# Optimization experiments

Hardware: AMD Instinct MI355X
Metric: run time of the kernel (lower is better)

## Reference

```python
import jax, jax.numpy as jnp
import numpy as np

THETA = 10000.0
D_K = 128
MAX_SEQ_LEN = 4096
BATCH, HEADS, SEQ = 4, 16, 4096


def _create_rotation_matrix(theta, d_k, max_seq_len):
    # Block-diagonal 2x2 rotation matrices, one per position: (max_seq_len, d_k, d_k)
    k = jnp.arange(d_k // 2)
    inv_freq = theta ** (-2.0 * k / d_k)                      # (d_k/2,)
    m = jnp.arange(max_seq_len, dtype=jnp.float32)
    angles = m[:, None] * inv_freq[None, :]                   # (S, d_k/2)
    c, s = jnp.cos(angles), jnp.sin(angles)
    i = 2 * k
    R = jnp.zeros((max_seq_len, d_k, d_k), dtype=jnp.float32)
    R = R.at[:, i, i].set(c)
    R = R.at[:, i, i + 1].set(-s)
    R = R.at[:, i + 1, i].set(s)
    R = R.at[:, i + 1, i + 1].set(c)
    return R


def setup_inputs() -> dict:
    key = jax.random.key(0)
    k1, = jax.random.split(key, 1)
    X = jax.random.normal(k1, (BATCH, HEADS, SEQ, D_K), dtype=jnp.float32)
    token_positions = jnp.arange(SEQ, dtype=jnp.int64 if jax.config.jax_enable_x64 else jnp.int32)
    rotation_matrix = _create_rotation_matrix(THETA, D_K, MAX_SEQ_LEN)
    return {"X": X, "token_positions": token_positions, "rotation_matrix": rotation_matrix}


def reference(X, token_positions, rotation_matrix):
    # Gather per-position d_k x d_k rotation matrices, then apply as a matmul:
    # out[..., s, j] = sum_i R[pos[s], j, i] * X[..., s, i]
    R = rotation_matrix[token_positions]                      # (seq, d_k, d_k)
    return jnp.einsum('sji,bhsi->bhsj', R, X)
```

## Files before the change

kernel.cpp:

```cpp
#include <hip/hip_runtime.h>
#include <stdint.h>

__global__ __launch_bounds__(256) void rope_fused(
        const float* __restrict__ X,
        const float* __restrict__ R,
        const int* __restrict__ pos,
        float* __restrict__ out,
        int seq, int bh) {
    __shared__ float cs[128];

    const int s = blockIdx.x;
    const int t = threadIdx.x;

    const long p = (long)pos[s];
    const float* rp = R + p * 16384;
    if (t < 64) {
        cs[2 * t] = rp[258 * t];
    } else if (t < 128) {
        int k = t - 64;
        cs[2 * k + 1] = rp[258 * k + 128];
    }
    __syncthreads();

    const int d4 = t & 31;
    const float4 c4 = *(const float4*)(cs + (d4 << 2));

    const long rstride = (long)seq * 128;
    const float* Xs = X + (long)s * 128 + (d4 << 2);
    float*       Os = out + (long)s * 128 + (d4 << 2);

    const int nvec = bh * 32;
#pragma unroll 4
    for (int idx = t; idx < nvec; idx += 256) {
        const int row = idx >> 5;
        const long e = (long)row * rstride;
        float4 x = *(const float4*)(Xs + e);
        float4 o;
        o.x = c4.x * x.x - c4.y * x.y;
        o.y = c4.y * x.x + c4.x * x.y;
        o.z = c4.z * x.z - c4.w * x.w;
        o.w = c4.w * x.z + c4.z * x.w;
        *(float4*)(Os + e) = o;
    }
}

extern "C" void kernel_launch(void* const* d_in, const int* in_sizes, int n_in,
                              void* d_out, int out_size, void* d_ws, size_t ws_size,
                              hipStream_t stream) {
    const float* X   = (const float*)d_in[0];
    const int*   pos = (const int*)d_in[1];
    const float* R   = (const float*)d_in[2];
    float* out       = (float*)d_out;

    const long n   = (long)in_sizes[0];
    const int  seq = in_sizes[1];
    const int  bh  = (int)(n / ((long)seq * 128));

    rope_fused<<<seq, 256, 0, stream>>>(X, R, pos, out, seq, bh);
}
```

Baseline: 433.2 us.

## Split RoPE into cos/sin table build and flat contiguous apply kernel

Measured after the change: 423.1 us. 2.3% less time.

```diff
diff --git a/kernel.cpp b/kernel.cpp
--- a/kernel.cpp
+++ b/kernel.cpp
@@ -1,47 +1,58 @@
 #include <hip/hip_runtime.h>
 #include <stdint.h>
 
-__global__ __launch_bounds__(256) void rope_fused(
-        const float* __restrict__ X,
+__global__ __launch_bounds__(256) void build_cs_table(
         const float* __restrict__ R,
         const int* __restrict__ pos,
+        float* __restrict__ tab, int total) {
+    int idx = blockIdx.x * blockDim.x + threadIdx.x;
+    if (idx >= total) return;
+    int s = idx >> 7;
+    int j = idx & 127;
+    int k = j >> 1;
+    int is_sin = j & 1;
+    long p = (long)pos[s];
+    tab[idx] = R[p * 16384 + 258 * k + (is_sin ? 128 : 0)];
+}
+
+__global__ __launch_bounds__(256) void rope_apply_pow2(
+        const float* __restrict__ X,
+        const float* __restrict__ tab,
         float* __restrict__ out,
-        int seq, int bh) {
-    __shared__ float cs[128];
+        int smask, int n4) {
+    int i = blockIdx.x * blockDim.x + threadIdx.x;
+    if (i >= n4) return;
+    int s  = (i >> 5) & smask;
+    int d0 = (i & 31) << 2;
 
-    const int s = blockIdx.x;
-    const int t = threadIdx.x;
+    float4 x  = *(const float4*)(X + ((long)i << 2));
+    float4 cs = *(const float4*)(tab + s * 128 + d0);
+    float4 o;
+    o.x = cs.x * x.x - cs.y * x.y;
+    o.y = cs.y * x.x + cs.x * x.y;
+    o.z = cs.z * x.z - cs.w * x.w;
+    o.w = cs.w * x.z + cs.z * x.w;
+    *(float4*)(out + ((long)i << 2)) = o;
+}
 
-    const long p = (long)pos[s];
-    const float* rp = R + p * 16384;
-    if (t < 64) {
-        cs[2 * t] = rp[258 * t];
-    } else if (t < 128) {
-        int k = t - 64;
-        cs[2 * k + 1] = rp[258 * k + 128];
-    }
-    __syncthreads();
+__global__ __launch_bounds__(256) void rope_apply_any(
+        const float* __restrict__ X,
+        const float* __restrict__ tab,
+        float* __restrict__ out,
+        int seq, int n4) {
+    int i = blockIdx.x * blockDim.x + threadIdx.x;
+    if (i >= n4) return;
+    int s  = (i >> 5) % seq;
+    int d0 = (i & 31) << 2;
 
-    const int d4 = t & 31;
-    const float4 c4 = *(const float4*)(cs + (d4 << 2));
-
-    const long rstride = (long)seq * 128;
-    const float* Xs = X + (long)s * 128 + (d4 << 2);
-    float*       Os = out + (long)s * 128 + (d4 << 2);
-
-    const int nvec = bh * 32;
-#pragma unroll 4
-    for (int idx = t; idx < nvec; idx += 256) {
-        const int row = idx >> 5;
-        const long e = (long)row * rstride;
-        float4 x = *(const float4*)(Xs + e);
-        float4 o;
-        o.x = c4.x * x.x - c4.y * x.y;
-        o.y = c4.y * x.x + c4.x * x.y;
-        o.z = c4.z * x.z - c4.w * x.w;
-        o.w = c4.w * x.z + c4.z * x.w;
-        *(float4*)(Os + e) = o;
-    }
+    float4 x  = *(const float4*)(X + ((long)i << 2));
+    float4 cs = *(const float4*)(tab + s * 128 + d0);
+    float4 o;
+    o.x = cs.x * x.x - cs.y * x.y;
+    o.y = cs.y * x.x + cs.x * x.y;
+    o.z = cs.z * x.z - cs.w * x.w;
+    o.w = cs.w * x.z + cs.z * x.w;
+    *(float4*)(out + ((long)i << 2)) = o;
 }
 
 extern "C" void kernel_launch(void* const* d_in, const int* in_sizes, int n_in,
@@ -51,10 +62,21 @@
     const int*   pos = (const int*)d_in[1];
     const float* R   = (const float*)d_in[2];
     float* out       = (float*)d_out;
+    float* tab       = (float*)d_ws;
 
-    const long n   = (long)in_sizes[0];
-    const int  seq = in_sizes[1];
-    const int  bh  = (int)(n / ((long)seq * 128));
+    const int n   = in_sizes[0];
+    const int seq = in_sizes[1];
+    const int n4  = n >> 2;
 
-    rope_fused<<<seq, 256, 0, stream>>>(X, R, pos, out, seq, bh);
+    const int blk = 256;
+    const int total = seq * 128;
+    build_cs_table<<<(total + blk - 1) / blk, blk, 0, stream>>>(R, pos, tab, total);
+
+    if ((seq & (seq - 1)) == 0) {
+        rope_apply_pow2<<<(n4 + blk - 1) / blk, blk, 0, stream>>>(
+            X, tab, out, seq - 1, n4);
+    } else {
+        rope_apply_any<<<(n4 + blk - 1) / blk, blk, 0, stream>>>(
+            X, tab, out, seq, n4);
+    }
 }
```
